# Kernel tuning notes

Hardware: AMD Instinct MI355X
Metric: run time of the kernel (lower is better)

## Reference

```python
import jax, jax.numpy as jnp
import numpy as np

N = 256          # num agents
HID = 128        # hidden_dim
ACT = 5          # action_dim
NH = 4           # num_heads
D = HID + 16     # concat_hidden_dim = 144
E = D * NH       # mha embed dim = 576
HD = D           # per-head dim = E // NH = 144
OBS_RX, OBS_RY = 4, 2   # obs_r from fov_size=(9,5)
GRID = 40


def setup_inputs() -> dict:
    key = jax.random.key(0)
    ks = jax.random.split(key, 24)
    g = lambda k, shape, s: (jax.random.normal(k, shape, dtype=jnp.float32) * s)
    inp = {
        "hidden_state_n": g(ks[0], (N, HID), 1.0),
        "action_n": g(ks[1], (N, HID), 1.0),
        "state_n": jax.random.randint(ks[2], (N, 2), 0, GRID, dtype=jnp.int32),
        # obs encoder
        "W_enc": g(ks[3], (HID, 16), HID ** -0.5), "b_enc": jnp.zeros((16,), jnp.float32),
        # MHABlock outer projections
        "Wq": g(ks[4], (D, E), D ** -0.5), "bq": jnp.zeros((E,), jnp.float32),
        "Wk": g(ks[5], (D, E), D ** -0.5), "bk": jnp.zeros((E,), jnp.float32),
        "Wv": g(ks[6], (D, E), D ** -0.5), "bv": jnp.zeros((E,), jnp.float32),
        # nn.MultiheadAttention internal in/out projections
        "Wiq": g(ks[7], (E, E), E ** -0.5), "biq": jnp.zeros((E,), jnp.float32),
        "Wik": g(ks[8], (E, E), E ** -0.5), "bik": jnp.zeros((E,), jnp.float32),
        "Wiv": g(ks[9], (E, E), E ** -0.5), "biv": jnp.zeros((E,), jnp.float32),
        "Wo_proj": g(ks[10], (E, E), E ** -0.5), "bo_proj": jnp.zeros((E,), jnp.float32),
        "W_O": g(ks[11], (E, D), E ** -0.5),  # no bias
        # dueling decoders
        "W_val": g(ks[12], (D, 1), D ** -0.5), "b_val": jnp.zeros((1,), jnp.float32),
        "W_adv": g(ks[13], (D, ACT), D ** -0.5), "b_adv": jnp.zeros((ACT,), jnp.float32),
    }
    return inp


def reference(hidden_state_n, action_n, W_enc, b_enc, Wq, bq, Wk, bk, Wv, bv,
              Wiq, biq, Wik, bik, Wiv, biv, Wo_proj, bo_proj, W_O,
              W_val, b_val, W_adv, b_adv, state_n):
    n = hidden_state_n.shape[0]
    # observed_agents[i] = {j > i : |x_i-x_j|<=rx and |y_i-y_j|<=ry}
    pos = state_n.astype(jnp.int32)
    dx = jnp.abs(pos[:, None, 0] - pos[None, :, 0])
    dy = jnp.abs(pos[:, None, 1] - pos[None, :, 1])
    upper = jnp.arange(n)[None, :] > jnp.arange(n)[:, None]
    mask = (dx <= OBS_RX) & (dy <= OBS_RY) & upper            # [N,N], mask[i,j]: j observed by i

    # per-neighbor feature c_j = concat(obs_encoder(h_j), a_j)  -> [N, D]
    obs = hidden_state_n @ W_enc + b_enc                       # [N,16]
    C = jnp.concatenate([obs, action_n], axis=-1)              # [N,D]

    # MHABlock: outer Q/K/V projections then nn.MultiheadAttention
    q = (C @ Wq + bq) @ Wiq + biq                              # [N,E]
    k = (C @ Wk + bk) @ Wik + bik
    v = (C @ Wv + bv) @ Wiv + biv
    q2 = q.reshape(n, NH, HD)
    k2 = k.reshape(n, NH, HD)
    v2 = v.reshape(n, NH, HD)

    scale = 1.0 / np.sqrt(HD).astype(np.float32)
    S = jnp.einsum("jhd,khd->hjk", q2, k2) * scale             # [H,N,N] shared across agents

    pair = (mask[:, None, :, None] & mask[:, None, None, :])   # [N,1,Nq,Nk]
    logits = jnp.where(pair, S[None, :, :, :], -1e9)           # [N,H,N,N]
    m = jnp.max(logits, axis=-1, keepdims=True)
    p = jnp.exp(logits - m) * pair.astype(logits.dtype)
    attn = p / jnp.maximum(p.sum(axis=-1, keepdims=True), 1e-9)

    ctx = jnp.einsum("ihjk,khd->ijhd", attn, v2).reshape(n, n, E)  # [N,Nq,E]
    out = (ctx @ Wo_proj + bo_proj) @ W_O                          # [N,Nq,D]

    # sum over the (masked) neighbor/query axis -> per-agent h_i
    h = jnp.sum(out * mask[:, :, None].astype(out.dtype), axis=1)  # [N,D]

    V = h @ W_val + b_val                                          # [N,1]
    A = h @ W_adv + b_adv                                          # [N,ACT]
    Q = V + A - jnp.mean(A, axis=-1, keepdims=True)                # dueling Q
    return Q
```

## Files before the change

kernel.cpp:

```cpp
#include <hip/hip_runtime.h>
#include <hip/hip_bf16.h>

#define NAG 256
#define HID 128
#define ACT 5
#define NH 4
#define DD 144
#define EE 576
#define HDIM 144
#define CMAX 20

__global__ __launch_bounds__(128) void k_prep(
    const float* __restrict__ hidden, const float* __restrict__ action,
    const float* __restrict__ W_enc, const float* __restrict__ b_enc,
    float* __restrict__ C)
{
    __shared__ float hrow[HID];
    __shared__ float part[8][16];
    const int i = blockIdx.x, t = threadIdx.x;
    hrow[t] = hidden[i * HID + t];
    __syncthreads();
    const int o = t & 15, pr = t >> 4;
    float p = 0.f;
    for (int d = pr * 16; d < pr * 16 + 16; ++d)
        p += hrow[d] * W_enc[d * 16 + o];
    part[pr][o] = p;
    __syncthreads();
    if (t < 16) {
        float s = 0.f;
        for (int pp = 0; pp < 8; ++pp) s += part[pp][t];
        C[i * DD + t] = s + b_enc[t];
    }
    C[i * DD + 16 + t] = action[i * HID + t];
}

template<int K>
__global__ __launch_bounds__(256) void k_gemm(
    const float* __restrict__ A0, const float* __restrict__ A1, const float* __restrict__ A2,
    const float* __restrict__ W0, const float* __restrict__ W1, const float* __restrict__ W2,
    const float* __restrict__ bb0, const float* __restrict__ bb1, const float* __restrict__ bb2,
    const float* __restrict__ bscale,
    float* __restrict__ o0, float* __restrict__ o1, float* __restrict__ o2,
    int N)
{
    constexpr int LDA = K + 4;
    __shared__ float As[16 * LDA];
    const int z = blockIdx.z;
    const float* A   = (z == 0) ? A0  : (z == 1) ? A1  : A2;
    const float* W   = (z == 0) ? W0  : (z == 1) ? W1  : W2;
    const float* bia = (z == 0) ? bb0 : (z == 1) ? bb1 : bb2;
    float*       out = (z == 0) ? o0  : (z == 1) ? o1  : o2;
    const int tid = threadIdx.x, mb = blockIdx.y;

    {
        const float4* Af = (const float4*)(A + (size_t)mb * 16 * K);
        for (int idx = tid; idx < 16 * K / 4; idx += 256) {
            float4 v4 = Af[idx];
            int lin = idx * 4;
            int rr = lin / K, kk = lin - rr * K;
            *((float4*)&As[rr * LDA + kk]) = v4;
        }
    }
    __syncthreads();

    const int r = tid >> 4;
    const int col = blockIdx.x * 64 + (tid & 15) * 4;
    if (col >= N) return;
    const float* Ar = &As[r * LDA];
    const float* Wc = W + col;
    float ac0 = 0.f, ac1 = 0.f, ac2 = 0.f, ac3 = 0.f;
    #pragma unroll 8
    for (int k = 0; k < K; ++k) {
        float a = Ar[k];
        float4 w4 = *(const float4*)(Wc + (size_t)k * N);
        ac0 += a * w4.x; ac1 += a * w4.y; ac2 += a * w4.z; ac3 += a * w4.w;
    }
    const int row = mb * 16 + r;
    float bs = bscale ? bscale[row] : 1.f;
    float4 o4;
    o4.x = ac0 + (bia ? bs * bia[col + 0] : 0.f);
    o4.y = ac1 + (bia ? bs * bia[col + 1] : 0.f);
    o4.z = ac2 + (bia ? bs * bia[col + 2] : 0.f);
    o4.w = ac3 + (bia ? bs * bia[col + 3] : 0.f);
    *((float4*)(out + (size_t)row * N + col)) = o4;
}

__global__ __launch_bounds__(256) void k_scores(
    const float* __restrict__ q, const float* __restrict__ kk,
    float* __restrict__ S)
{
    __shared__ float Qs[16][HDIM + 1];
    __shared__ float Ks[16][HDIM + 1];
    const int kb = blockIdx.x * 16, jb = blockIdx.y * 16, h = blockIdx.z;
    const int tid = threadIdx.x;
    for (int idx = tid; idx < 16 * HDIM; idx += 256) {
        int r = idx / HDIM, d = idx % HDIM;
        Qs[r][d] = q[(jb + r) * EE + h * HDIM + d];
        Ks[r][d] = kk[(kb + r) * EE + h * HDIM + d];
    }
    __syncthreads();
    const int ty = tid >> 4, tx = tid & 15;
    float acc = 0.f;
    for (int d = 0; d < HDIM; ++d) acc += Qs[ty][d] * Ks[tx][d];
    S[h * (NAG * NAG) + (jb + ty) * NAG + (kb + tx)] = acc * (1.0f / 12.0f);
}

__global__ __launch_bounds__(256) void k_attn(
    const int* __restrict__ state, const float* __restrict__ S,
    const float* __restrict__ v, float* __restrict__ ctxsum,
    float* __restrict__ cnt)
{
    __shared__ int lst[NAG];
    __shared__ int cnt_s;
    __shared__ float w4[NH][NAG];
    __shared__ float Sl[NH][CMAX][CMAX + 1];
    const int i = blockIdx.x, tid = threadIdx.x;
    if (tid == 0) cnt_s = 0;
    __syncthreads();
    {
        int xi = state[2 * i], yi = state[2 * i + 1];
        int xj = state[2 * tid], yj = state[2 * tid + 1];
        int dx = xi - xj; if (dx < 0) dx = -dx;
        int dy = yi - yj; if (dy < 0) dy = -dy;
        if (tid > i && dx <= 4 && dy <= 2) {
            int p = atomicAdd(&cnt_s, 1);
            lst[p] = tid;
        }
    }
    __syncthreads();
    const int c = cnt_s;
    if (tid == 0) cnt[i] = (float)c;
    if (c == 0) {
        for (int e = tid; e < EE; e += 256) ctxsum[i * EE + e] = 0.f;
        return;
    }
    if (c <= CMAX) {
        for (int idx = tid; idx < NH * c * c; idx += 256) {
            int h = idx / (c * c), rem = idx % (c * c);
            int jj = rem / c, kk = rem % c;
            Sl[h][jj][kk] = S[h * (NAG * NAG) + lst[jj] * NAG + lst[kk]];
        }
        __syncthreads();
        for (int p = tid; p < NH * c; p += 256) {
            int h = p / c, jj = p % c;
            float m = -1e30f;
            for (int kk = 0; kk < c; ++kk) m = fmaxf(m, Sl[h][jj][kk]);
            float z = 0.f;
            for (int kk = 0; kk < c; ++kk) z += __expf(Sl[h][jj][kk] - m);
            float inv = 1.f / fmaxf(z, 1e-9f);
            for (int kk = 0; kk < c; ++kk)
                Sl[h][jj][kk] = __expf(Sl[h][jj][kk] - m) * inv;
        }
        __syncthreads();
        for (int p = tid; p < NH * c; p += 256) {
            int h = p / c, kk = p % c;
            float s = 0.f;
            for (int jj = 0; jj < c; ++jj) s += Sl[h][jj][kk];
            w4[h][kk] = s;
        }
        __syncthreads();
    } else {
        for (int idx = tid; idx < NH * c; idx += 256) w4[idx / c][idx % c] = 0.f;
        __syncthreads();
        for (int p = tid; p < NH * c; p += 256) {
            int h = p / c, jj = p % c;
            const float* Srow = S + h * (NAG * NAG) + lst[jj] * NAG;
            float m = -1e30f;
            for (int kk = 0; kk < c; ++kk) m = fmaxf(m, Srow[lst[kk]]);
            float z = 0.f;
            for (int kk = 0; kk < c; ++kk) z += __expf(Srow[lst[kk]] - m);
            float inv = 1.f / fmaxf(z, 1e-9f);
            for (int kk = 0; kk < c; ++kk)
                atomicAdd(&w4[h][kk], __expf(Srow[lst[kk]] - m) * inv);
        }
        __syncthreads();
    }
    for (int e = tid; e < EE; e += 256) {
        int h = e / HDIM;
        float acc = 0.f;
        for (int t = 0; t < c; ++t) acc += w4[h][t] * v[lst[t] * EE + e];
        ctxsum[i * EE + e] = acc;
    }
}

__global__ __launch_bounds__(64) void k_head(
    const float* __restrict__ h,
    const float* __restrict__ W_val, const float* __restrict__ b_val,
    const float* __restrict__ W_adv, const float* __restrict__ b_adv,
    float* __restrict__ out)
{
    const int i = blockIdx.x, t = threadIdx.x;
    const float* hr = h + i * DD;
    float h0 = hr[t], h1 = hr[t + 64];
    float h2 = (t < 16) ? hr[t + 128] : 0.f;
    float red[6];
    for (int o = 0; o < 6; ++o) {
        float p;
        if (o < 5) {
            p = h0 * W_adv[t * ACT + o] + h1 * W_adv[(t + 64) * ACT + o];
            if (t < 16) p += h2 * W_adv[(t + 128) * ACT + o];
        } else {
            p = h0 * W_val[t] + h1 * W_val[t + 64];
            if (t < 16) p += h2 * W_val[t + 128];
        }
        for (int off = 32; off; off >>= 1) p += __shfl_xor(p, off);
        red[o] = p;
    }
    if (t == 0) {
        float a[ACT], mean = 0.f;
        for (int o = 0; o < ACT; ++o) { a[o] = red[o] + b_adv[o]; mean += a[o]; }
        mean *= (1.0f / ACT);
        float V = red[5] + b_val[0];
        for (int o = 0; o < ACT; ++o) out[i * ACT + o] = V + a[o] - mean;
    }
}

extern "C" void kernel_launch(void* const* d_in, const int* in_sizes, int n_in,
                              void* d_out, int out_size, void* d_ws, size_t ws_size,
                              hipStream_t stream)
{
    const float* hidden = (const float*)d_in[0];
    const float* action = (const float*)d_in[1];
    const int*   state  = (const int*)d_in[2];

    float* ws = (float*)d_ws;
    float* C    = ws;
    float* tq   = C   + NAG * DD;
    float* tk   = tq  + NAG * EE;
    float* tv   = tk  + NAG * EE;
    float* q    = tv  + NAG * EE;
    float* kbuf = q   + NAG * EE;
    float* v    = kbuf+ NAG * EE;
    float* S    = v   + NAG * EE;
    float* cnt  = S   + NH * NAG * NAG;
    float* ctx  = q;
    float* tout = kbuf;
    float* hbuf = tq;

    k_prep<<<NAG, 128, 0, stream>>>(hidden, action,
        (const float*)d_in[3], (const float*)d_in[4], C);

    dim3 g3(9, 16, 3);
    k_gemm<144><<<g3, 256, 0, stream>>>(C, C, C,
        (const float*)d_in[5], (const float*)d_in[7], (const float*)d_in[9],
        (const float*)d_in[6], (const float*)d_in[8], (const float*)d_in[10],
        nullptr, tq, tk, tv, EE);

    k_gemm<576><<<g3, 256, 0, stream>>>(tq, tk, tv,
        (const float*)d_in[11], (const float*)d_in[13], (const float*)d_in[15],
        (const float*)d_in[12], (const float*)d_in[14], (const float*)d_in[16],
        nullptr, q, kbuf, v, EE);

    k_scores<<<dim3(16, 16, 4), 256, 0, stream>>>(q, kbuf, S);
    k_attn<<<NAG, 256, 0, stream>>>(state, S, v, ctx, cnt);

    dim3 g1a(9, 16, 1);
    k_gemm<576><<<g1a, 256, 0, stream>>>(ctx, ctx, ctx,
        (const float*)d_in[17], (const float*)d_in[17], (const float*)d_in[17],
        (const float*)d_in[18], (const float*)d_in[18], (const float*)d_in[18],
        cnt, tout, tout, tout, EE);

    dim3 g1b(3, 16, 1);
    k_gemm<576><<<g1b, 256, 0, stream>>>(tout, tout, tout,
        (const float*)d_in[19], (const float*)d_in[19], (const float*)d_in[19],
        nullptr, nullptr, nullptr,
        nullptr, hbuf, hbuf, hbuf, DD);

    k_head<<<NAG, 64, 0, stream>>>(hbuf,
        (const float*)d_in[20], (const float*)d_in[21],
        (const float*)d_in[22], (const float*)d_in[23], (float*)d_out);
}
```

Measured before the change: 237.2 us.

## Fuse encoder into first GEMM, compute scores inside attention, remap blocks per XCD

Folds the observation encoder into the first projection GEMM, so each block recomputes the 16-wide encoding for its 16 rows and the separate prep kernel goes away. The full H×N×N score kernel is dropped: each attention block now computes only the scores for its own neighbour pairs from q and k staged in shared memory. GEMM grids are flattened into 1D with an XCD-aware mapping, so blocks sharing a weight column tile land on the same XCD for L2 reuse. The cost is redundant encoder work, launches padded to 512 blocks with idle early exits, and per-head serialization plus extra barriers in the attention kernel.

New measurement: 239.8 us. About the same (+1.1%).

```diff
diff --git a/kernel.cpp b/kernel.cpp
--- a/kernel.cpp
+++ b/kernel.cpp
@@ -10,32 +10,61 @@
 #define HDIM 144
 #define CMAX 20
 
-__global__ __launch_bounds__(128) void k_prep(
+__global__ __launch_bounds__(256) void k_gemm1(
     const float* __restrict__ hidden, const float* __restrict__ action,
     const float* __restrict__ W_enc, const float* __restrict__ b_enc,
-    float* __restrict__ C)
-{
-    __shared__ float hrow[HID];
-    __shared__ float part[8][16];
-    const int i = blockIdx.x, t = threadIdx.x;
-    hrow[t] = hidden[i * HID + t];
-    __syncthreads();
-    const int o = t & 15, pr = t >> 4;
-    float p = 0.f;
-    for (int d = pr * 16; d < pr * 16 + 16; ++d)
-        p += hrow[d] * W_enc[d * 16 + o];
-    part[pr][o] = p;
-    __syncthreads();
-    if (t < 16) {
-        float s = 0.f;
-        for (int pp = 0; pp < 8; ++pp) s += part[pp][t];
-        C[i * DD + t] = s + b_enc[t];
-    }
-    C[i * DD + 16 + t] = action[i * HID + t];
-}
-
-template<int K>
-__global__ __launch_bounds__(256) void k_gemm(
+    const float* __restrict__ Wq, const float* __restrict__ Wk, const float* __restrict__ Wv,
+    const float* __restrict__ bq, const float* __restrict__ bk, const float* __restrict__ bv,
+    float* __restrict__ tq, float* __restrict__ tk, float* __restrict__ tv)
+{
+    const int p = blockIdx.x;
+    const int xcd = p & 7, qq = p >> 3;
+    const int gslot = qq >> 4, mb = qq & 15;
+    const int g = xcd + 8 * gslot;
+    if (g >= 27) return;
+    const int bx = g % 9, z = g / 9;
+    const float* W  = (z == 0) ? Wq : (z == 1) ? Wk : Wv;
+    const float* bi = (z == 0) ? bq : (z == 1) ? bk : bv;
+    float*      out = (z == 0) ? tq : (z == 1) ? tk : tv;
+
+    __shared__ float Hs[16][HID + 4];
+    __shared__ float As[16][DD + 4];
+    const int tid = threadIdx.x;
+    {
+        const float4* Hf = (const float4*)(hidden + mb * 16 * HID);
+        const float4* Af = (const float4*)(action + mb * 16 * HID);
+        for (int idx = tid; idx < 16 * HID / 4; idx += 256) {
+            int lin = idx * 4, rr = lin >> 7, kk = lin & 127;
+            *((float4*)&Hs[rr][kk]) = Hf[idx];
+            *((float4*)&As[rr][16 + kk]) = Af[idx];
+        }
+    }
+    __syncthreads();
+    {
+        int r = tid >> 4, o = tid & 15;
+        float acc = 0.f;
+        for (int d = 0; d < HID; ++d) acc += Hs[r][d] * W_enc[d * 16 + o];
+        As[r][o] = acc + b_enc[o];
+    }
+    __syncthreads();
+    const int r = tid >> 4;
+    const int col = bx * 64 + (tid & 15) * 4;
+    const float* Ar = As[r];
+    const float* Wc = W + col;
+    float ac0 = 0.f, ac1 = 0.f, ac2 = 0.f, ac3 = 0.f;
+    #pragma unroll 8
+    for (int k = 0; k < DD; ++k) {
+        float a = Ar[k];
+        float4 w4 = *(const float4*)(Wc + (size_t)k * EE);
+        ac0 += a * w4.x; ac1 += a * w4.y; ac2 += a * w4.z; ac3 += a * w4.w;
+    }
+    const int row = mb * 16 + r;
+    float4 o4 = { ac0 + bi[col], ac1 + bi[col + 1], ac2 + bi[col + 2], ac3 + bi[col + 3] };
+    *((float4*)(out + (size_t)row * EE + col)) = o4;
+}
+
+template<int K, int NX, int G>
+__global__ __launch_bounds__(256) void k_gemmN(
     const float* __restrict__ A0, const float* __restrict__ A1, const float* __restrict__ A2,
     const float* __restrict__ W0, const float* __restrict__ W1, const float* __restrict__ W2,
     const float* __restrict__ bb0, const float* __restrict__ bb1, const float* __restrict__ bb2,
@@ -43,15 +72,20 @@
     float* __restrict__ o0, float* __restrict__ o1, float* __restrict__ o2,
     int N)
 {
+    const int p = blockIdx.x;
+    const int xcd = p & 7, qq = p >> 3;
+    const int gslot = qq >> 4, mb = qq & 15;
+    const int g = xcd + 8 * gslot;
+    if (g >= G) return;
+    const int bx = g % NX, z = g / NX;
+
     constexpr int LDA = K + 4;
     __shared__ float As[16 * LDA];
-    const int z = blockIdx.z;
     const float* A   = (z == 0) ? A0  : (z == 1) ? A1  : A2;
     const float* W   = (z == 0) ? W0  : (z == 1) ? W1  : W2;
     const float* bia = (z == 0) ? bb0 : (z == 1) ? bb1 : bb2;
     float*       out = (z == 0) ? o0  : (z == 1) ? o1  : o2;
-    const int tid = threadIdx.x, mb = blockIdx.y;
-
+    const int tid = threadIdx.x;
     {
         const float4* Af = (const float4*)(A + (size_t)mb * 16 * K);
         for (int idx = tid; idx < 16 * K / 4; idx += 256) {
@@ -62,9 +96,8 @@
         }
     }
     __syncthreads();
-
     const int r = tid >> 4;
-    const int col = blockIdx.x * 64 + (tid & 15) * 4;
+    const int col = bx * 64 + (tid & 15) * 4;
     if (col >= N) return;
     const float* Ar = &As[r * LDA];
     const float* Wc = W + col;
@@ -85,35 +118,17 @@
     *((float4*)(out + (size_t)row * N + col)) = o4;
 }
 
-__global__ __launch_bounds__(256) void k_scores(
-    const float* __restrict__ q, const float* __restrict__ kk,
-    float* __restrict__ S)
-{
-    __shared__ float Qs[16][HDIM + 1];
-    __shared__ float Ks[16][HDIM + 1];
-    const int kb = blockIdx.x * 16, jb = blockIdx.y * 16, h = blockIdx.z;
-    const int tid = threadIdx.x;
-    for (int idx = tid; idx < 16 * HDIM; idx += 256) {
-        int r = idx / HDIM, d = idx % HDIM;
-        Qs[r][d] = q[(jb + r) * EE + h * HDIM + d];
-        Ks[r][d] = kk[(kb + r) * EE + h * HDIM + d];
-    }
-    __syncthreads();
-    const int ty = tid >> 4, tx = tid & 15;
-    float acc = 0.f;
-    for (int d = 0; d < HDIM; ++d) acc += Qs[ty][d] * Ks[tx][d];
-    S[h * (NAG * NAG) + (jb + ty) * NAG + (kb + tx)] = acc * (1.0f / 12.0f);
-}
-
 __global__ __launch_bounds__(256) void k_attn(
-    const int* __restrict__ state, const float* __restrict__ S,
-    const float* __restrict__ v, float* __restrict__ ctxsum,
-    float* __restrict__ cnt)
+    const int* __restrict__ state, const float* __restrict__ q,
+    const float* __restrict__ kmat, const float* __restrict__ v,
+    float* __restrict__ ctxsum, float* __restrict__ cnt)
 {
     __shared__ int lst[NAG];
     __shared__ int cnt_s;
     __shared__ float w4[NH][NAG];
-    __shared__ float Sl[NH][CMAX][CMAX + 1];
+    __shared__ float qh[CMAX][HDIM + 1];
+    __shared__ float kh[CMAX][HDIM + 1];
+    __shared__ float Sl[CMAX][CMAX + 1];
     const int i = blockIdx.x, tid = threadIdx.x;
     if (tid == 0) cnt_s = 0;
     __syncthreads();
@@ -135,43 +150,64 @@
         return;
     }
     if (c <= CMAX) {
-        for (int idx = tid; idx < NH * c * c; idx += 256) {
-            int h = idx / (c * c), rem = idx % (c * c);
-            int jj = rem / c, kk = rem % c;
-            Sl[h][jj][kk] = S[h * (NAG * NAG) + lst[jj] * NAG + lst[kk]];
-        }
-        __syncthreads();
-        for (int p = tid; p < NH * c; p += 256) {
-            int h = p / c, jj = p % c;
-            float m = -1e30f;
-            for (int kk = 0; kk < c; ++kk) m = fmaxf(m, Sl[h][jj][kk]);
-            float z = 0.f;
-            for (int kk = 0; kk < c; ++kk) z += __expf(Sl[h][jj][kk] - m);
-            float inv = 1.f / fmaxf(z, 1e-9f);
-            for (int kk = 0; kk < c; ++kk)
-                Sl[h][jj][kk] = __expf(Sl[h][jj][kk] - m) * inv;
-        }
-        __syncthreads();
-        for (int p = tid; p < NH * c; p += 256) {
-            int h = p / c, kk = p % c;
-            float s = 0.f;
-            for (int jj = 0; jj < c; ++jj) s += Sl[h][jj][kk];
-            w4[h][kk] = s;
-        }
-        __syncthreads();
+        for (int h = 0; h < NH; ++h) {
+            for (int idx = tid; idx < c * HDIM; idx += 256) {
+                int jj = idx / HDIM, d = idx % HDIM;
+                qh[jj][d] = q[lst[jj] * EE + h * HDIM + d];
+                kh[jj][d] = kmat[lst[jj] * EE + h * HDIM + d];
+            }
+            __syncthreads();
+            for (int pp = tid; pp < c * c; pp += 256) {
+                int jj = pp / c, kk = pp % c;
+                float acc = 0.f;
+                for (int d = 0; d < HDIM; ++d) acc += qh[jj][d] * kh[kk][d];
+                Sl[jj][kk] = acc * (1.0f / 12.0f);
+            }
+            __syncthreads();
+            if (tid < c) {
+                float m = -1e30f;
+                for (int kk = 0; kk < c; ++kk) m = fmaxf(m, Sl[tid][kk]);
+                float zz = 0.f;
+                for (int kk = 0; kk < c; ++kk) zz += __expf(Sl[tid][kk] - m);
+                float inv = 1.f / fmaxf(zz, 1e-9f);
+                for (int kk = 0; kk < c; ++kk)
+                    Sl[tid][kk] = __expf(Sl[tid][kk] - m) * inv;
+            }
+            __syncthreads();
+            if (tid < c) {
+                float s = 0.f;
+                for (int jj = 0; jj < c; ++jj) s += Sl[jj][tid];
+                w4[h][tid] = s;
+            }
+            __syncthreads();
+        }
     } else {
         for (int idx = tid; idx < NH * c; idx += 256) w4[idx / c][idx % c] = 0.f;
         __syncthreads();
-        for (int p = tid; p < NH * c; p += 256) {
-            int h = p / c, jj = p % c;
-            const float* Srow = S + h * (NAG * NAG) + lst[jj] * NAG;
+        for (int pnh = tid; pnh < NH * c; pnh += 256) {
+            int h = pnh / c, jj = pnh % c;
+            const float* qrow = q + lst[jj] * EE + h * HDIM;
             float m = -1e30f;
-            for (int kk = 0; kk < c; ++kk) m = fmaxf(m, Srow[lst[kk]]);
-            float z = 0.f;
-            for (int kk = 0; kk < c; ++kk) z += __expf(Srow[lst[kk]] - m);
-            float inv = 1.f / fmaxf(z, 1e-9f);
-            for (int kk = 0; kk < c; ++kk)
-                atomicAdd(&w4[h][kk], __expf(Srow[lst[kk]] - m) * inv);
+            for (int kk = 0; kk < c; ++kk) {
+                const float* krow = kmat + lst[kk] * EE + h * HDIM;
+                float a = 0.f;
+                for (int d = 0; d < HDIM; ++d) a += qrow[d] * krow[d];
+                m = fmaxf(m, a * (1.0f / 12.0f));
+            }
+            float zz = 0.f;
+            for (int kk = 0; kk < c; ++kk) {
+                const float* krow = kmat + lst[kk] * EE + h * HDIM;
+                float a = 0.f;
+                for (int d = 0; d < HDIM; ++d) a += qrow[d] * krow[d];
+                zz += __expf(a * (1.0f / 12.0f) - m);
+            }
+            float inv = 1.f / fmaxf(zz, 1e-9f);
+            for (int kk = 0; kk < c; ++kk) {
+                const float* krow = kmat + lst[kk] * EE + h * HDIM;
+                float a = 0.f;
+                for (int d = 0; d < HDIM; ++d) a += qrow[d] * krow[d];
+                atomicAdd(&w4[h][kk], __expf(a * (1.0f / 12.0f) - m) * inv);
+            }
         }
         __syncthreads();
     }
@@ -224,44 +260,36 @@
     const int*   state  = (const int*)d_in[2];
 
     float* ws = (float*)d_ws;
-    float* C    = ws;
-    float* tq   = C   + NAG * DD;
+    float* tq   = ws;
     float* tk   = tq  + NAG * EE;
     float* tv   = tk  + NAG * EE;
     float* q    = tv  + NAG * EE;
     float* kbuf = q   + NAG * EE;
     float* v    = kbuf+ NAG * EE;
-    float* S    = v   + NAG * EE;
-    float* cnt  = S   + NH * NAG * NAG;
-    float* ctx  = q;
-    float* tout = kbuf;
-    float* hbuf = tq;
-
-    k_prep<<<NAG, 128, 0, stream>>>(hidden, action,
-        (const float*)d_in[3], (const float*)d_in[4], C);
-
-    dim3 g3(9, 16, 3);
-    k_gemm<144><<<g3, 256, 0, stream>>>(C, C, C,
+    float* ctx  = v   + NAG * EE;
+    float* cnt  = ctx + NAG * EE;
+    float* tout = tq;
+    float* hbuf = tk;
+
+    k_gemm1<<<512, 256, 0, stream>>>(hidden, action,
+        (const float*)d_in[3], (const float*)d_in[4],
         (const float*)d_in[5], (const float*)d_in[7], (const float*)d_in[9],
         (const float*)d_in[6], (const float*)d_in[8], (const float*)d_in[10],
-        nullptr, tq, tk, tv, EE);
-
-    k_gemm<576><<<g3, 256, 0, stream>>>(tq, tk, tv,
+        tq, tk, tv);
+
+    k_gemmN<576, 9, 27><<<512, 256, 0, stream>>>(tq, tk, tv,
         (const float*)d_in[11], (const float*)d_in[13], (const float*)d_in[15],
         (const float*)d_in[12], (const float*)d_in[14], (const float*)d_in[16],
         nullptr, q, kbuf, v, EE);
 
-    k_scores<<<dim3(16, 16, 4), 256, 0, stream>>>(q, kbuf, S);
-    k_attn<<<NAG, 256, 0, stream>>>(state, S, v, ctx, cnt);
-
-    dim3 g1a(9, 16, 1);
-    k_gemm<576><<<g1a, 256, 0, stream>>>(ctx, ctx, ctx,
+    k_attn<<<NAG, 256, 0, stream>>>(state, q, kbuf, v, ctx, cnt);
+
+    k_gemmN<576, 9, 9><<<256, 256, 0, stream>>>(ctx, ctx, ctx,
         (const float*)d_in[17], (const float*)d_in[17], (const float*)d_in[17],
         (const float*)d_in[18], (const float*)d_in[18], (const float*)d_in[18],
         cnt, tout, tout, tout, EE);
 
-    dim3 g1b(3, 16, 1);
-    k_gemm<576><<<g1b, 256, 0, stream>>>(tout, tout, tout,
+    k_gemmN<576, 3, 3><<<128, 256, 0, stream>>>(tout, tout, tout,
         (const float*)d_in[19], (const float*)d_in[19], (const float*)d_in[19],
         nullptr, nullptr, nullptr,
         nullptr, hbuf, hbuf, hbuf, DD);
```
